# Performance work log

Hardware: AMD Instinct MI355X
Metric: run time of the kernel (lower is better)

Reference implementation:

```python
import jax, jax.numpy as jnp
import numpy as np

OUT_F = 4096
IN_F = 4096
NNZ_ROW = 204  # round(0.05 * IN_F) outliers kept per row


def setup_inputs() -> dict:
    key = jax.random.key(0)
    k_x, k_w, k_s, k_v, k_i = jax.random.split(key, 5)
    x = jax.random.normal(k_x, (4096, IN_F), dtype=jnp.float32)
    # packed int4 pairs: each byte holds two offset-nibbles (value+8 in [1,15]); any byte works for reference math
    base_packed = jax.random.randint(k_w, (OUT_F, IN_F // 2), 0, 256, dtype=jnp.int32)
    # per-row scales = row_absmax/7 > 0
    scales = jax.random.uniform(k_s, (OUT_F,), dtype=jnp.float32, minval=0.001, maxval=0.05)
    nnz = OUT_F * NNZ_ROW
    ortho_vals = (jax.random.normal(k_v, (nnz,), dtype=jnp.float32) * 0.01).astype(jnp.float16)
    # CSR: NNZ_ROW sorted column indices per row
    idx = jax.random.randint(k_i, (OUT_F, NNZ_ROW), 0, IN_F, dtype=jnp.int32)
    ortho_indices = jnp.sort(idx, axis=1).reshape(-1)
    ortho_ptr = (jnp.arange(OUT_F + 1, dtype=jnp.int32) * NNZ_ROW)
    return {
        "x": x,
        "base_packed": base_packed,
        "scales": scales,
        "ortho_vals": ortho_vals,
        "ortho_indices": ortho_indices,
        "ortho_ptr": ortho_ptr,
    }


def reference(x, base_packed, scales, ortho_vals, ortho_indices, ortho_ptr):
    out_f = base_packed.shape[0]
    in_f = base_packed.shape[1] * 2
    alpha = 1.0

    # --- dequantize packed int4 base weights: low nibble -> even cols, high nibble -> odd cols ---
    p = base_packed.astype(jnp.int32)
    low = (p & 0xF) - 8            # [out, in/2]
    high = ((p >> 4) & 0xF) - 8    # [out, in/2]
    w_int = jnp.stack([low, high], axis=-1).reshape(out_f, in_f)  # interleaved [l0,h0,l1,h1,...]
    w_base = w_int.astype(jnp.float32) * scales[:, None]          # [out, in]

    # --- CSR sparse outlier residual, scattered to dense for the reference GEMM ---
    nnz = ortho_vals.shape[0]
    row_ids = jnp.searchsorted(ortho_ptr, jnp.arange(nnz, dtype=jnp.int32), side="right") - 1
    w_sparse = jnp.zeros((out_f, in_f), jnp.float32).at[row_ids, ortho_indices].add(
        ortho_vals.astype(jnp.float32)
    )

    w = w_base + alpha * w_sparse
    x_flat = x.reshape(-1, in_f).astype(jnp.float32)
    out = x_flat @ w.T  # [tokens, out]
    out = out.reshape(x.shape[:-1] + (out_f,))
    return out.astype(x.dtype)
```

## Files before the change

kernel.cpp:

```cpp
#include <hip/hip_runtime.h>
#include <hip/hip_fp16.h>

typedef __attribute__((ext_vector_type(4))) int i32x4;

#define GLOBAL_AS __attribute__((address_space(1)))
#define LDS_AS __attribute__((address_space(3)))

static __device__ __forceinline__ void gload16(const void* g, void* l) {
    __builtin_amdgcn_global_load_lds((const GLOBAL_AS void*)g, (LDS_AS void*)l, 16, 0, 0);
}

#define SBAR() __builtin_amdgcn_s_barrier()
#define WAITVM(N) asm volatile("s_waitcnt vmcnt(" #N ")" ::: "memory")

static __device__ __forceinline__ int q8(float v, float inv) {
    int q = (int)rintf(v * inv);
    q = q > 127 ? 127 : q;
    q = q < -127 ? -127 : q;
    return q & 255;
}

__global__ __launch_bounds__(256) void prep_kernel(
    const int* __restrict__ packed,
    const float* __restrict__ scales,
    const void* __restrict__ vals,
    const int* __restrict__ idxs,
    const int* __restrict__ ptr,
    int* __restrict__ Wq,
    const float* __restrict__ x,
    int* __restrict__ Xq,
    float* __restrict__ sw,
    float* __restrict__ sx)
{
    const int tid = threadIdx.x;
    __shared__ float smax[4];
    if (blockIdx.x >= 4096) {
        const int row = blockIdx.x - 4096;
        const float4* xp4 = (const float4*)(x + (size_t)row * 4096);
        float4 v0 = xp4[tid], v1 = xp4[tid + 256], v2 = xp4[tid + 512], v3 = xp4[tid + 768];
        float am = fabsf(v0.x);
        am = fmaxf(am, fabsf(v0.y)); am = fmaxf(am, fabsf(v0.z)); am = fmaxf(am, fabsf(v0.w));
        am = fmaxf(am, fabsf(v1.x)); am = fmaxf(am, fabsf(v1.y)); am = fmaxf(am, fabsf(v1.z)); am = fmaxf(am, fabsf(v1.w));
        am = fmaxf(am, fabsf(v2.x)); am = fmaxf(am, fabsf(v2.y)); am = fmaxf(am, fabsf(v2.z)); am = fmaxf(am, fabsf(v2.w));
        am = fmaxf(am, fabsf(v3.x)); am = fmaxf(am, fabsf(v3.y)); am = fmaxf(am, fabsf(v3.z)); am = fmaxf(am, fabsf(v3.w));
        for (int o = 32; o; o >>= 1) am = fmaxf(am, __shfl_xor(am, o));
        if ((tid & 63) == 0) smax[tid >> 6] = am;
        __syncthreads();
        am = fmaxf(fmaxf(smax[0], smax[1]), fmaxf(smax[2], smax[3]));
        const float sc_ = am > 1e-30f ? am / 127.0f : 0.0f;
        const float inv = am > 1e-30f ? 127.0f / am : 0.0f;
        if (tid == 0) sx[row] = sc_;
        int* orow = Xq + (size_t)row * 1024;
        orow[tid]       = q8(v0.x,inv) | (q8(v0.y,inv)<<8) | (q8(v0.z,inv)<<16) | (q8(v0.w,inv)<<24);
        orow[tid + 256] = q8(v1.x,inv) | (q8(v1.y,inv)<<8) | (q8(v1.z,inv)<<16) | (q8(v1.w,inv)<<24);
        orow[tid + 512] = q8(v2.x,inv) | (q8(v2.y,inv)<<8) | (q8(v2.z,inv)<<16) | (q8(v2.w,inv)<<24);
        orow[tid + 768] = q8(v3.x,inv) | (q8(v3.y,inv)<<8) | (q8(v3.z,inv)<<16) | (q8(v3.w,inv)<<24);
        return;
    }
    __shared__ float sp[4096];
    __shared__ int sdet[3];
    const int row = blockIdx.x;
    float4* sp4 = (float4*)sp;
    const float4 z4 = make_float4(0.f, 0.f, 0.f, 0.f);
    for (int i = tid; i < 1024; i += 256) sp4[i] = z4;
    {
        const int wvp = tid >> 6, ln = tid & 63;
        if (wvp < 3) {
            int c = 0;
            for (int i = ln; i < 192; i += 64) {
                float a;
                if (wvp == 0) a = fabsf(((const float*)vals)[i]);
                else if (wvp == 1) a = fabsf(__half2float(((const __half*)vals)[i]));
                else { union { unsigned u; float fv; } cc;
                       cc.u = ((unsigned)((const unsigned short*)vals)[i]) << 16;
                       a = fabsf(cc.fv); }
                c += (a >= 1e-5f && a <= 0.5f) ? 1 : 0;
            }
            for (int o = 32; o; o >>= 1) c += __shfl_down(c, o);
            if (ln == 0) sdet[wvp] = c;
        }
    }
    __syncthreads();
    const int kind = (sdet[0] >= sdet[1] && sdet[0] >= sdet[2]) ? 0 : (sdet[1] >= sdet[2] ? 1 : 2);
    const int s = ptr[row], e = ptr[row + 1];
    if (kind == 0) {
        const float* vf = (const float*)vals;
        for (int i = s + tid; i < e; i += 256) atomicAdd(&sp[idxs[i]], vf[i]);
    } else if (kind == 1) {
        const __half* vh = (const __half*)vals;
        for (int i = s + tid; i < e; i += 256) atomicAdd(&sp[idxs[i]], __half2float(vh[i]));
    } else {
        const unsigned short* vb = (const unsigned short*)vals;
        for (int i = s + tid; i < e; i += 256) {
            union { unsigned u; float fv; } c; c.u = ((unsigned)vb[i]) << 16;
            atomicAdd(&sp[idxs[i]], c.fv);
        }
    }
    __syncthreads();
    const float scr = scales[row];
    const int* prow = packed + (size_t)row * 2048;
    float am = 0.0f;
    for (int j = tid; j < 2048; j += 256) {
        const int p = prow[j];
        const float lo = (float)((p & 0xF) - 8) * scr + sp[2 * j];
        const float hi = (float)(((p >> 4) & 0xF) - 8) * scr + sp[2 * j + 1];
        sp[2 * j] = lo; sp[2 * j + 1] = hi;
        am = fmaxf(am, fmaxf(fabsf(lo), fabsf(hi)));
    }
    for (int o = 32; o; o >>= 1) am = fmaxf(am, __shfl_xor(am, o));
    if ((tid & 63) == 0) smax[tid >> 6] = am;
    __syncthreads();
    am = fmaxf(fmaxf(smax[0], smax[1]), fmaxf(smax[2], smax[3]));
    const float sc2 = am > 1e-30f ? am / 127.0f : 0.0f;
    const float inv2 = am > 1e-30f ? 127.0f / am : 0.0f;
    if (tid == 0) sw[row] = sc2;
    int* wrow = Wq + (size_t)row * 1024;
    for (int j = tid; j < 1024; j += 256) {
        const float* c4 = sp + 4 * j;
        wrow[j] = q8(c4[0],inv2) | (q8(c4[1],inv2)<<8) | (q8(c4[2],inv2)<<16) | (q8(c4[3],inv2)<<24);
    }
}

__global__ __launch_bounds__(512, 2) void gemm_bt_kernel(
    const signed char* __restrict__ A,
    const signed char* __restrict__ B,
    const float* __restrict__ sx,
    const float* __restrict__ sw,
    float* __restrict__ C)
{
    constexpr int KB = 4096;
    constexpr int N = 4096;
    constexpr int NT = 32;
    __shared__ __attribute__((aligned(128))) char smem[163840];

    const int tid = threadIdx.x;
    const int lane = tid & 63;
    const int wv = tid >> 6;
    const int bid = (blockIdx.x & 7) * 32 + (blockIdx.x >> 3);
    const int bm = bid >> 4;
    const int bn = bid & 15;

    const int grow = tid >> 3;
    const int sg = (tid & 7) ^ (grow & 7);
    const signed char* ag = A + (size_t)(bm * 256 + grow) * KB + sg * 16;
    const signed char* bg = B + (size_t)(bn * 256 + grow) * KB + sg * 16;

#define STA(R, KTB, SLOT)                                                              \
    gload16(ag + (size_t)((R) * 64) * KB + (KTB),                                      \
            smem + (SLOT) * 32768 + (R) * 8192 + wv * 1024);
#define STB(R, KTB, SLOT)                                                              \
    gload16(bg + (size_t)((R) * 64) * KB + (KTB),                                      \
            smem + (SLOT) * 32768 + (R) * 8192 + wv * 1024);

    const int wr = wv >> 2, wc = wv & 3;
    const int rowa = wr * 128 + (lane & 15);
    const int rowb = wc * 64 + (lane & 15);
    const int khw = lane >> 4;
    const int rx = lane & 7;

#define LDA4(DST, MH, KK, SLOT)                                                        \
    {                                                                                  \
        _Pragma("unroll") for (int m = 0; m < 4; ++m) {                                \
            const int row_ = rowa + (MH) * 64 + m * 16;                                \
            DST[m] = *(const i32x4*)(smem + (SLOT) * 32768 + row_ * 128 +              \
                                     (((((KK) << 2) + khw) ^ rx) << 4));               \
        }                                                                              \
    }
#define LDB4(DST, KK, SLOT)                                                            \
    {                                                                                  \
        _Pragma("unroll") for (int n = 0; n < 4; ++n) {                                \
            const int row_ = rowb + n * 16;                                            \
            DST[n] = *(const i32x4*)(smem + (SLOT) * 32768 + row_ * 128 +              \
                                     (((((KK) << 2) + khw) ^ rx) << 4));               \
        }                                                                              \
    }
#define MFMA16(AF, BF, MH)                                                             \
    {                                                                                  \
        _Pragma("unroll") for (int m = 0; m < 4; ++m)                                  \
            _Pragma("unroll") for (int n = 0; n < 4; ++n)                              \
                acc[(MH) * 4 + m][n] = __builtin_amdgcn_mfma_i32_16x16x64_i8(          \
                    AF[m], BF[n], acc[(MH) * 4 + m][n], 0, 0, 0);                      \
    }

    i32x4 acc[8][4];
#pragma unroll
    for (int m = 0; m < 8; ++m)
#pragma unroll
        for (int n = 0; n < 4; ++n) acc[m][n] = (i32x4)0;

#pragma unroll
    for (int r = 0; r < 4; ++r) STA(r, 0, 0);
#pragma unroll
    for (int r = 0; r < 4; ++r) STB(r, 0, 1);
#pragma unroll
    for (int r = 0; r < 4; ++r) STA(r, 128, 2);

    int sA = 0, sB = 1, sB1 = 3, sA2 = 4;
    for (int t = 0; t < NT; ++t) {
        const int ktn = (t + 1) * 128;
        const int ktn2 = (t + 2) * 128;
        const bool s1 = (t + 1 < NT), s2 = (t + 2 < NT);
        if (s1) { WAITVM(4); } else { WAITVM(0); }
        SBAR();
        __builtin_amdgcn_sched_barrier(0);

        i32x4 af0[4], af1[4], af2[4], af3[4], bf0[4], bf1[4];
        LDA4(af0, 0, 0, sA); LDB4(bf0, 0, sB);
        LDA4(af1, 1, 0, sA);
        if (s1) { STB(0, ktn, sB1); STB(1, ktn, sB1); }
        MFMA16(af0, bf0, 0);
        LDA4(af2, 0, 1, sA); LDB4(bf1, 1, sB);
        if (s1) { STB(2, ktn, sB1); STB(3, ktn, sB1); }
        MFMA16(af1, bf0, 1);
        LDA4(af3, 1, 1, sA);
        if (s2) { STA(0, ktn2, sA2); STA(1, ktn2, sA2); }
        MFMA16(af2, bf1, 0);
        if (s2) { STA(2, ktn2, sA2); STA(3, ktn2, sA2); }
        MFMA16(af3, bf1, 1);

        sA += 2; if (sA >= 5) sA -= 5;
        sB += 2; if (sB >= 5) sB -= 5;
        sB1 += 2; if (sB1 >= 5) sB1 -= 5;
        sA2 += 2; if (sA2 >= 5) sA2 -= 5;
    }

    const int crow0 = bm * 256 + wr * 128 + (lane >> 4) * 4;
    const int ccol0 = bn * 256 + wc * 64 + (lane & 15);
#pragma unroll
    for (int n = 0; n < 4; ++n) {
        const float swn = sw[ccol0 + n * 16];
#pragma unroll
        for (int m = 0; m < 8; ++m)
#pragma unroll
            for (int r = 0; r < 4; ++r) {
                const int row_ = crow0 + m * 16 + r;
                C[(size_t)row_ * N + ccol0 + n * 16] =
                    sx[row_] * swn * (float)acc[m][n][r];
            }
    }
}

extern "C" void kernel_launch(void* const* d_in, const int* in_sizes, int n_in,
                              void* d_out, int out_size, void* d_ws, size_t ws_size,
                              hipStream_t stream) {
    const float* x        = (const float*)d_in[0];
    const int* packed     = (const int*)d_in[1];
    const float* scales   = (const float*)d_in[2];
    const void* vals      = (const void*)d_in[3];
    const int* idxs       = (const int*)d_in[4];
    const int* ptr        = (const int*)d_in[5];
    float* out            = (float*)d_out;

    char* ws = (char*)d_ws;
    int* Wq   = (int*)ws;
    int* Xq   = (int*)(ws + (size_t)16 * 1024 * 1024);
    float* sw = (float*)(ws + (size_t)32 * 1024 * 1024);
    float* sx = (float*)(ws + (size_t)32 * 1024 * 1024 + 16384);

    prep_kernel<<<8192, 256, 0, stream>>>(packed, scales, vals, idxs, ptr,
                                          Wq, x, Xq, sw, sx);
    gemm_bt_kernel<<<256, 512, 0, stream>>>((const signed char*)Xq,
                                            (const signed char*)Wq, sx, sw, out);
}
```

Measured before the change: 102.2 us.

## Shrink int8 GEMM tiles to 128x128 with simple double-buffered K=64 pipeline

Replaces the 256x256 tile, 512-thread GEMM, which used a five-slot LDS ring and staggered A/B prefetch, with 128x128 tiles on 256 threads. It uses a K step of 64, two LDS buffers of 16 KB, and 1024 blocks. Smaller LDS use and launch bounds of (256,4) allow more resident blocks per CU and better load balance across CUs. In exchange, each block reuses data less (arithmetic intensity halves), global traffic rises, and each K step issues fewer MFMAs between barriers. MFMA issue priority is also raised with s_setprio.

Result: slower. 128.5 us (+25.7%).

```diff
diff --git a/kernel.cpp b/kernel.cpp
--- a/kernel.cpp
+++ b/kernel.cpp
@@ -121,7 +121,7 @@
     }
 }
 
-__global__ __launch_bounds__(512, 2) void gemm_bt_kernel(
+__global__ __launch_bounds__(256, 4) void gemm_bt_kernel(
     const signed char* __restrict__ A,
     const signed char* __restrict__ B,
     const float* __restrict__ sx,
@@ -130,107 +130,96 @@
 {
     constexpr int KB = 4096;
     constexpr int N = 4096;
-    constexpr int NT = 32;
-    __shared__ __attribute__((aligned(128))) char smem[163840];
+    constexpr int NT = 64;
+    __shared__ __attribute__((aligned(128))) char smem[32768];
 
     const int tid = threadIdx.x;
     const int lane = tid & 63;
     const int wv = tid >> 6;
-    const int bid = (blockIdx.x & 7) * 32 + (blockIdx.x >> 3);
-    const int bm = bid >> 4;
-    const int bn = bid & 15;
-
-    const int grow = tid >> 3;
-    const int sg = (tid & 7) ^ (grow & 7);
-    const signed char* ag = A + (size_t)(bm * 256 + grow) * KB + sg * 16;
-    const signed char* bg = B + (size_t)(bn * 256 + grow) * KB + sg * 16;
-
-#define STA(R, KTB, SLOT)                                                              \
-    gload16(ag + (size_t)((R) * 64) * KB + (KTB),                                      \
-            smem + (SLOT) * 32768 + (R) * 8192 + wv * 1024);
-#define STB(R, KTB, SLOT)                                                              \
-    gload16(bg + (size_t)((R) * 64) * KB + (KTB),                                      \
-            smem + (SLOT) * 32768 + (R) * 8192 + wv * 1024);
-
-    const int wr = wv >> 2, wc = wv & 3;
-    const int rowa = wr * 128 + (lane & 15);
+    const int bid = (blockIdx.x & 7) * 128 + (blockIdx.x >> 3);
+    const int bm = bid >> 5;
+    const int bn = bid & 31;
+
+    const int grow = tid >> 2;
+    const int sg = (tid & 3) ^ ((grow >> 1) & 3);
+    const signed char* ag = A + (size_t)(bm * 128 + grow) * KB + sg * 16;
+    const signed char* bg = B + (size_t)(bn * 128 + grow) * KB + sg * 16;
+
+#define STAGE(R, KT, BUF)                                                              \
+    {                                                                                  \
+        if ((R) < 2)                                                                   \
+            gload16(ag + (size_t)((R) * 64) * KB + (KT),                               \
+                    smem + (BUF) * 16384 + (R) * 4096 + wv * 1024);                    \
+        else                                                                           \
+            gload16(bg + (size_t)(((R) - 2) * 64) * KB + (KT),                         \
+                    smem + (BUF) * 16384 + 8192 + ((R) - 2) * 4096 + wv * 1024);       \
+    }
+
+    const int wr = wv >> 1, wc = wv & 1;
+    const int rowa = wr * 64 + (lane & 15);
     const int rowb = wc * 64 + (lane & 15);
     const int khw = lane >> 4;
-    const int rx = lane & 7;
-
-#define LDA4(DST, MH, KK, SLOT)                                                        \
+    const int fx = (lane >> 1) & 3;
+
+#define LDA4(DST, BUF)                                                                 \
     {                                                                                  \
         _Pragma("unroll") for (int m = 0; m < 4; ++m) {                                \
-            const int row_ = rowa + (MH) * 64 + m * 16;                                \
-            DST[m] = *(const i32x4*)(smem + (SLOT) * 32768 + row_ * 128 +              \
-                                     (((((KK) << 2) + khw) ^ rx) << 4));               \
+            const int row_ = rowa + m * 16;                                            \
+            DST[m] = *(const i32x4*)(smem + (BUF) * 16384 + row_ * 64 +                \
+                                     ((khw ^ fx) << 4));                               \
         }                                                                              \
     }
-#define LDB4(DST, KK, SLOT)                                                            \
+#define LDB4(DST, BUF)                                                                 \
     {                                                                                  \
         _Pragma("unroll") for (int n = 0; n < 4; ++n) {                                \
             const int row_ = rowb + n * 16;                                            \
-            DST[n] = *(const i32x4*)(smem + (SLOT) * 32768 + row_ * 128 +              \
-                                     (((((KK) << 2) + khw) ^ rx) << 4));               \
+            DST[n] = *(const i32x4*)(smem + (BUF) * 16384 + 8192 + row_ * 64 +         \
+                                     ((khw ^ fx) << 4));                               \
         }                                                                              \
     }
-#define MFMA16(AF, BF, MH)                                                             \
-    {                                                                                  \
-        _Pragma("unroll") for (int m = 0; m < 4; ++m)                                  \
-            _Pragma("unroll") for (int n = 0; n < 4; ++n)                              \
-                acc[(MH) * 4 + m][n] = __builtin_amdgcn_mfma_i32_16x16x64_i8(          \
-                    AF[m], BF[n], acc[(MH) * 4 + m][n], 0, 0, 0);                      \
-    }
-
-    i32x4 acc[8][4];
-#pragma unroll
-    for (int m = 0; m < 8; ++m)
+
+    i32x4 acc[4][4];
+#pragma unroll
+    for (int m = 0; m < 4; ++m)
 #pragma unroll
         for (int n = 0; n < 4; ++n) acc[m][n] = (i32x4)0;
 
 #pragma unroll
-    for (int r = 0; r < 4; ++r) STA(r, 0, 0);
-#pragma unroll
-    for (int r = 0; r < 4; ++r) STB(r, 0, 1);
-#pragma unroll
-    for (int r = 0; r < 4; ++r) STA(r, 128, 2);
-
-    int sA = 0, sB = 1, sB1 = 3, sA2 = 4;
+    for (int r = 0; r < 4; ++r) STAGE(r, 0, 0);
+
     for (int t = 0; t < NT; ++t) {
-        const int ktn = (t + 1) * 128;
-        const int ktn2 = (t + 2) * 128;
-        const bool s1 = (t + 1 < NT), s2 = (t + 2 < NT);
-        if (s1) { WAITVM(4); } else { WAITVM(0); }
+        const int cur = t & 1, nxt = cur ^ 1;
+        const int ktn = (t + 1) * 64;
+        if (t + 1 < NT) {
+#pragma unroll
+            for (int r = 0; r < 4; ++r) STAGE(r, ktn, nxt);
+            WAITVM(4);
+        } else {
+            WAITVM(0);
+        }
         SBAR();
         __builtin_amdgcn_sched_barrier(0);
 
-        i32x4 af0[4], af1[4], af2[4], af3[4], bf0[4], bf1[4];
-        LDA4(af0, 0, 0, sA); LDB4(bf0, 0, sB);
-        LDA4(af1, 1, 0, sA);
-        if (s1) { STB(0, ktn, sB1); STB(1, ktn, sB1); }
-        MFMA16(af0, bf0, 0);
-        LDA4(af2, 0, 1, sA); LDB4(bf1, 1, sB);
-        if (s1) { STB(2, ktn, sB1); STB(3, ktn, sB1); }
-        MFMA16(af1, bf0, 1);
-        LDA4(af3, 1, 1, sA);
-        if (s2) { STA(0, ktn2, sA2); STA(1, ktn2, sA2); }
-        MFMA16(af2, bf1, 0);
-        if (s2) { STA(2, ktn2, sA2); STA(3, ktn2, sA2); }
-        MFMA16(af3, bf1, 1);
-
-        sA += 2; if (sA >= 5) sA -= 5;
-        sB += 2; if (sB >= 5) sB -= 5;
-        sB1 += 2; if (sB1 >= 5) sB1 -= 5;
-        sA2 += 2; if (sA2 >= 5) sA2 -= 5;
-    }
-
-    const int crow0 = bm * 256 + wr * 128 + (lane >> 4) * 4;
-    const int ccol0 = bn * 256 + wc * 64 + (lane & 15);
+        i32x4 af[4], bf[4];
+        LDA4(af, cur); LDB4(bf, cur);
+        __builtin_amdgcn_s_setprio(1);
+#pragma unroll
+        for (int m = 0; m < 4; ++m)
+#pragma unroll
+            for (int n = 0; n < 4; ++n)
+                acc[m][n] = __builtin_amdgcn_mfma_i32_16x16x64_i8(
+                    af[m], bf[n], acc[m][n], 0, 0, 0);
+        __builtin_amdgcn_s_setprio(0);
+        SBAR();
+    }
+
+    const int crow0 = bm * 128 + wr * 64 + (lane >> 4) * 4;
+    const int ccol0 = bn * 128 + wc * 64 + (lane & 15);
 #pragma unroll
     for (int n = 0; n < 4; ++n) {
         const float swn = sw[ccol0 + n * 16];
 #pragma unroll
-        for (int m = 0; m < 8; ++m)
+        for (int m = 0; m < 4; ++m)
 #pragma unroll
             for (int r = 0; r < 4; ++r) {
                 const int row_ = crow0 + m * 16 + r;
@@ -259,6 +248,6 @@
 
     prep_kernel<<<8192, 256, 0, stream>>>(packed, scales, vals, idxs, ptr,
                                           Wq, x, Xq, sw, sx);
-    gemm_bt_kernel<<<256, 512, 0, stream>>>((const signed char*)Xq,
-                                            (const signed char*)Wq, sx, sw, out);
-}
+    gemm_bt_kernel<<<1024, 256, 0, stream>>>((const signed char*)Xq,
+                                             (const signed char*)Wq, sx, sw, out);
+}
```
